# Optimization experiments

Measured on AMD Instinct MI355X. Metric: run time of the kernel, lower is better.

The kernel has to match this reference:

```python
import jax, jax.numpy as jnp
import numpy as np

B, LQ, H, NH, LK, N = 32, 256, 256, 8, 512, 8192
DH = H // NH
EPS = 1e-12

def layer_norm(x, g, b):
    m = x.mean(-1, keepdims=True)
    v = ((x - m) ** 2).mean(-1, keepdims=True)
    return (x - m) / jnp.sqrt(v + EPS) * g + b

def setup_inputs() -> dict:
    rs = np.random.RandomState(0)
    counts = rs.randint(LK // 2, LK + 1, size=B)  # ragged per-graph edge counts, max = LK
    E = int(counts.sum())
    edge_batch = jnp.asarray(np.repeat(np.arange(B), counts), jnp.int32)
    edge_pos = jnp.asarray(np.concatenate([np.arange(c) for c in counts]), jnp.int32)
    pad_mask = jnp.asarray((np.arange(LK)[None, :] < counts[:, None]).astype(np.float32))
    src = jnp.asarray(rs.randint(0, N, E), jnp.int32)
    dst = jnp.asarray(rs.randint(0, N, E), jnp.int32)
    ks = jax.random.split(jax.random.key(0), 16)
    def rn(i, shape, s=0.02):
        return jax.random.normal(ks[i], shape, jnp.float32) * s
    return dict(
        extended_attention_mask=jnp.zeros((B, 1, 1, LQ), jnp.float32),
        query=rn(0, (B, LQ, H), 1.0),
        rel_embedding_output=rn(1, (E, H), 1.0),
        graph_output=rn(2, (N, H), 1.0),
        src=src, dst=dst, edge_batch=edge_batch, edge_pos=edge_pos, pad_mask=pad_mask,
        Wq=rn(3, (H, H)), bq=jnp.zeros((H,), jnp.float32),
        Wk=rn(4, (2 * H, H)), bk=jnp.zeros((H,), jnp.float32),
        Wv=rn(5, (H, H)), bv=jnp.zeros((H,), jnp.float32),
        Wo=rn(6, (H, H)), bo=jnp.zeros((H,), jnp.float32),
        ln1_g=jnp.ones((H,), jnp.float32), ln1_b=jnp.zeros((H,), jnp.float32),
        W1=rn(7, (H, H)), b1=jnp.zeros((H,), jnp.float32),
        W2=rn(8, (H, H)), b2=jnp.zeros((H,), jnp.float32),
        ln2_g=jnp.ones((H,), jnp.float32), ln2_b=jnp.zeros((H,), jnp.float32),
    )

def reference(extended_attention_mask, query, rel_embedding_output, graph_output,
              src, dst, edge_batch, edge_pos, pad_mask,
              Wq, bq, Wk, bk, Wv, bv, Wo, bo, ln1_g, ln1_b,
              W1, b1, W2, b2, ln2_g, ln2_b):
    # --- memory_transform: edge gather + ragged pad (vectorized scatter) ---
    key_flat = jnp.concatenate([graph_output[src], rel_embedding_output], -1)  # [E, 2H]
    dst_flat = graph_output[dst]                                               # [E, H]
    key_pad = jnp.zeros((B, LK, 2 * H), key_flat.dtype).at[edge_batch, edge_pos].set(key_flat)
    val_pad = jnp.zeros((B, LK, H), dst_flat.dtype).at[edge_batch, edge_pos].set(dst_flat)
    cross_mask = (1.0 - pad_mask)[:, None, None, :] * -10000.0                 # [B,1,1,LK]
    # --- BidiAttention ---
    Q = (query @ Wq + bq).reshape(B, LQ, NH, DH)
    K = (key_pad @ Wk + bk).reshape(B, LK, NH, DH)
    V = (val_pad @ Wv + bv).reshape(B, LK, NH, DH)
    scores = jnp.einsum('bqhd,bkhd->bhqk', Q, K) / np.float32(np.sqrt(DH))
    pq = jax.nn.softmax(scores + cross_mask, axis=-1)
    query_ctx = jnp.einsum('bhqk,bkhd->bqhd', pq, V).reshape(B, LQ, H)
    pv = jax.nn.softmax(scores.transpose(0, 1, 3, 2) + extended_attention_mask, axis=-1)
    value_ctx = jnp.einsum('bhkq,bqhd->bkhd', pv, Q).reshape(B, LK, H)
    # --- RelAwareCross output / gate ---
    query_out = layer_norm(query_ctx @ Wo + bo + query, ln1_g, ln1_b)
    theta = jax.nn.sigmoid(value_ctx @ W1 + b1 + val_pad @ W2 + b2)
    value_new = layer_norm(theta * value_ctx + (1.0 - theta) * val_pad, ln2_g, ln2_b)
    # --- memory_update: unpad + scatter-mean by dst, replace rows with incoming edges ---
    val_edges = value_new[edge_batch, edge_pos]                                # [E, H]
    sums = jax.ops.segment_sum(val_edges, dst, num_segments=N)
    cnts = jax.ops.segment_sum(jnp.ones((val_edges.shape[0],), val_edges.dtype), dst, num_segments=N)
    mean = sums / jnp.maximum(cnts, 1.0)[:, None]
    graph_new = jnp.where((cnts > 0)[:, None], mean, graph_output)
    return (graph_new, query_out)
```

## Files before the change

### kernel.cpp

```cpp
#include <hip/hip_runtime.h>
#include <hip/hip_bf16.h>
#include <string.h>

#define B_ 32
#define LQ_ 256
#define H_ 256
#define NH_ 8
#define LK_ 512
#define N_ 8192
#define DH_ 32

typedef float floatx4 __attribute__((ext_vector_type(4)));
typedef short shortx8 __attribute__((ext_vector_type(8)));
typedef short shortx4 __attribute__((ext_vector_type(4)));

__device__ __forceinline__ short f2b(float f) {
    __hip_bfloat16 h = __float2bfloat16(f);
    short s;
    __builtin_memcpy(&s, &h, 2);
    return s;
}
__device__ __forceinline__ float b2f(short s) {
    unsigned u = ((unsigned)(unsigned short)s) << 16;
    float f;
    __builtin_memcpy(&f, &u, 4);
    return f;
}

#define LOG2E 1.44269504088896f
#define MFMA32(a, b, c) __builtin_amdgcn_mfma_f32_16x16x32_bf16(a, b, c, 0, 0, 0)
#define MFMA16(a, b, c) __builtin_amdgcn_mfma_f32_16x16x16bf16_1k(a, b, c, 0, 0, 0)

__global__ __launch_bounds__(256) void phase1(
    const float* __restrict__ graph, const float* __restrict__ rel,
    const int* __restrict__ src, const int* __restrict__ dst,
    const int* __restrict__ eb, const int* __restrict__ ep,
    const float* __restrict__ pad_mask,
    const float* __restrict__ Wq, const float* __restrict__ Wk,
    const float* __restrict__ Wv, const float* __restrict__ Wo,
    const float* __restrict__ W1, const float* __restrict__ W2,
    short* __restrict__ WT, short* __restrict__ key_pad,
    short* __restrict__ val_pad, int* __restrict__ head,
    int* __restrict__ row2e, int E) {
    const int bid = blockIdx.x, tid = threadIdx.x;
    if (bid < 8192) {
        int row = bid * 2 + (tid >> 7);
        int t = tid & 127;
        int b = row >> 9, p = row & 511;
        bool valid = pad_mask[row] > 0.5f;
        size_t krow = (size_t)row * 512;
        size_t vrow = (size_t)row * 256;
        int kc = t * 4, vc = t * 2;
        if (valid) {
            int lo = 0, hi = E;
            while (lo < hi) { int mid = (lo + hi) >> 1; if (eb[mid] < b) lo = mid + 1; else hi = mid; }
            int e = lo + p;
            int s = src[e], d = dst[e];
            const float* sp = (kc < 256) ? (graph + (size_t)s * 256 + kc)
                                         : (rel + (size_t)e * 256 + (kc - 256));
            float4 k4 = *(const float4*)sp;
            key_pad[krow + kc + 0] = f2b(k4.x);
            key_pad[krow + kc + 1] = f2b(k4.y);
            key_pad[krow + kc + 2] = f2b(k4.z);
            key_pad[krow + kc + 3] = f2b(k4.w);
            float2 v2 = *(const float2*)(graph + (size_t)d * 256 + vc);
            val_pad[vrow + vc + 0] = f2b(v2.x);
            val_pad[vrow + vc + 1] = f2b(v2.y);
        } else {
            *(long long*)&key_pad[krow + kc] = 0;
            *(int*)&val_pad[vrow + vc] = 0;
        }
    } else if (bid < 9984) {
        int i = (bid - 8192) * 256 + tid;
        const float* s;
        int K, loc;
        if (i < 65536) { s = Wq; K = 256; loc = i; }
        else if (i < 196608) { s = Wk; K = 512; loc = i - 65536; }
        else {
            int m = (i - 196608) >> 16;
            loc = (i - 196608) & 65535;
            K = 256;
            s = (m == 0) ? Wv : (m == 1) ? Wo : (m == 2) ? W1 : W2;
        }
        int n = loc / K, k = loc - n * K;
        WT[i] = f2b(s[(size_t)k * 256 + n]);
    } else {
        int i = (bid - 9984) * 256 + tid;
        if (i < 8192) head[i] = -1;
        for (int j = i; j < E; j += 8192)
            row2e[eb[j] * 512 + ep[j]] = j;
    }
}

__global__ __launch_bounds__(256) void phase2_gemm(
    const float* __restrict__ query, const short* __restrict__ key_pad,
    const short* __restrict__ val_pad, const short* __restrict__ WT,
    const float* __restrict__ bq, const float* __restrict__ bk,
    const float* __restrict__ bv,
    short* __restrict__ Qb, short* __restrict__ Kb,
    short* __restrict__ Vt, short* __restrict__ Qt) {
    __shared__ short As[128][40];
    __shared__ short Bs[128][40];
    const int tid = threadIdx.x;
    const int id = blockIdx.x;
    const float* Af = nullptr; const short* Ab = nullptr;
    const float* Bf = nullptr; const short* Bb = nullptr;
    const float* bias; short* C;
    size_t cbase; int cstride, K; bool biasM;
    if (id < 128) {
        int mt = id >> 1, nt = id & 1;
        Af = query + (size_t)(mt * 128) * 256; K = 256;
        Bb = WT + (size_t)(nt * 128) * 256;
        bias = bq + nt * 128; biasM = false;
        C = Qb; cbase = (size_t)(mt * 128) * 256 + nt * 128; cstride = 256;
    } else if (id < 384) {
        int t = id - 128; int mt = t >> 1, nt = t & 1;
        Ab = key_pad + (size_t)(mt * 128) * 512; K = 512;
        Bb = WT + 65536 + (size_t)(nt * 128) * 512;
        bias = bk + nt * 128; biasM = false;
        C = Kb; cbase = (size_t)(mt * 128) * 256 + nt * 128; cstride = 256;
    } else if (id < 640) {
        int t = id - 384; int b = t >> 3, ct = (t >> 2) & 1, nt = t & 3;
        Ab = WT + 196608 + (size_t)(ct * 128) * 256; K = 256;
        Bb = val_pad + ((size_t)(b * 512 + nt * 128)) * 256;
        bias = bv + ct * 128; biasM = true;
        C = Vt; cbase = ((size_t)(b * 256 + ct * 128)) * 512 + nt * 128; cstride = 512;
    } else {
        int t = id - 640; int b = t >> 2, ct = (t >> 1) & 1, qt = t & 1;
        Ab = WT + (size_t)(ct * 128) * 256; K = 256;
        Bf = query + ((size_t)(b * 256 + qt * 128)) * 256;
        bias = bq + ct * 128; biasM = true;
        C = Qt; cbase = ((size_t)(b * 256 + ct * 128)) * 256 + qt * 128; cstride = 256;
    }
    const int w = tid >> 6, lane = tid & 63;
    const int R0 = (w >> 1) * 64, C0 = (w & 1) * 64;
    const int lm = lane & 15, quad = lane >> 4;
    const int sr = tid >> 1, skq = (tid & 1) * 16;

    floatx4 acc[4][4];
#pragma unroll
    for (int i = 0; i < 4; i++)
#pragma unroll
        for (int j = 0; j < 4; j++) acc[i][j] = {0.f, 0.f, 0.f, 0.f};

    for (int kc = 0; kc < K; kc += 32) {
        if (Af) {
            const float* ap = Af + (size_t)sr * K + kc + skq;
            float4 a1 = *(const float4*)ap, a2 = *(const float4*)(ap + 4);
            float4 a3 = *(const float4*)(ap + 8), a4 = *(const float4*)(ap + 12);
            As[sr][skq + 0] = f2b(a1.x); As[sr][skq + 1] = f2b(a1.y);
            As[sr][skq + 2] = f2b(a1.z); As[sr][skq + 3] = f2b(a1.w);
            As[sr][skq + 4] = f2b(a2.x); As[sr][skq + 5] = f2b(a2.y);
            As[sr][skq + 6] = f2b(a2.z); As[sr][skq + 7] = f2b(a2.w);
            As[sr][skq + 8] = f2b(a3.x); As[sr][skq + 9] = f2b(a3.y);
            As[sr][skq + 10] = f2b(a3.z); As[sr][skq + 11] = f2b(a3.w);
            As[sr][skq + 12] = f2b(a4.x); As[sr][skq + 13] = f2b(a4.y);
            As[sr][skq + 14] = f2b(a4.z); As[sr][skq + 15] = f2b(a4.w);
        } else {
            const short* ap = Ab + (size_t)sr * K + kc + skq;
            *(shortx8*)&As[sr][skq] = *(const shortx8*)ap;
            *(shortx8*)&As[sr][skq + 8] = *(const shortx8*)(ap + 8);
        }
        if (Bf) {
            const float* bp = Bf + (size_t)sr * K + kc + skq;
            float4 a1 = *(const float4*)bp, a2 = *(const float4*)(bp + 4);
            float4 a3 = *(const float4*)(bp + 8), a4 = *(const float4*)(bp + 12);
            Bs[sr][skq + 0] = f2b(a1.x); Bs[sr][skq + 1] = f2b(a1.y);
            Bs[sr][skq + 2] = f2b(a1.z); Bs[sr][skq + 3] = f2b(a1.w);
            Bs[sr][skq + 4] = f2b(a2.x); Bs[sr][skq + 5] = f2b(a2.y);
            Bs[sr][skq + 6] = f2b(a2.z); Bs[sr][skq + 7] = f2b(a2.w);
            Bs[sr][skq + 8] = f2b(a3.x); Bs[sr][skq + 9] = f2b(a3.y);
            Bs[sr][skq + 10] = f2b(a3.z); Bs[sr][skq + 11] = f2b(a3.w);
            Bs[sr][skq + 12] = f2b(a4.x); Bs[sr][skq + 13] = f2b(a4.y);
            Bs[sr][skq + 14] = f2b(a4.z); Bs[sr][skq + 15] = f2b(a4.w);
        } else {
            const short* bp = Bb + (size_t)sr * K + kc + skq;
            *(shortx8*)&Bs[sr][skq] = *(const shortx8*)bp;
            *(shortx8*)&Bs[sr][skq + 8] = *(const shortx8*)(bp + 8);
        }
        __syncthreads();
        shortx8 af[4], bf[4];
#pragma unroll
        for (int i = 0; i < 4; i++) {
            af[i] = *(const shortx8*)&As[R0 + i * 16 + lm][quad * 8];
            bf[i] = *(const shortx8*)&Bs[C0 + i * 16 + lm][quad * 8];
        }
#pragma unroll
        for (int i = 0; i < 4; i++)
#pragma unroll
            for (int j = 0; j < 4; j++)
                acc[i][j] = MFMA32(af[i], bf[j], acc[i][j]);
        __syncthreads();
    }
#pragma unroll
    for (int i = 0; i < 4; i++) {
#pragma unroll
        for (int j = 0; j < 4; j++) {
            int gn = C0 + j * 16 + lm;
#pragma unroll
            for (int r = 0; r < 4; r++) {
                int gm = R0 + i * 16 + quad * 4 + r;
                float bvv = biasM ? bias[gm] : bias[gn];
                C[cbase + (size_t)gm * cstride + gn] = f2b(acc[i][j][r] + bvv);
            }
        }
    }
}

__global__ __launch_bounds__(512, 4) void phase3_attn(
    const short* __restrict__ Qm, const short* __restrict__ Km,
    const short* __restrict__ Vt, const short* __restrict__ Qt,
    const float* __restrict__ pad_mask, const float* __restrict__ ext,
    short* __restrict__ qctx, short* __restrict__ vctx) {
    __shared__ short SA[128][40];
    __shared__ short ST[32][136];
    const int tid = threadIdx.x;
    const int w = tid >> 6, lane = tid & 63;
    const int lm = lane & 15, quad = lane >> 4;
    const float scale2 = 0.17677669529663687f * LOG2E;
    const int id = blockIdx.x;

    if (id < 256) {
        const int b = id >> 3, h = id & 7;
        shortx8 bqf[2];
        bqf[0] = *(const shortx8*)(Qm + ((size_t)(b * 256 + w * 32 + lm)) * 256 + h * 32 + quad * 8);
        bqf[1] = *(const shortx8*)(Qm + ((size_t)(b * 256 + w * 32 + 16 + lm)) * 256 + h * 32 + quad * 8);
        floatx4 oacc[2][2] = {{{0.f,0.f,0.f,0.f},{0.f,0.f,0.f,0.f}},
                              {{0.f,0.f,0.f,0.f},{0.f,0.f,0.f,0.f}}};
        float psum[2] = {0.f, 0.f};
        const floatx4* pmp = (const floatx4*)(pad_mask + b * 512);
        for (int kc = 0; kc < 512; kc += 128) {
            if (tid < 256) {
                int r = tid >> 1, dq = (tid & 1) * 16;
                const short* kp = Km + ((size_t)(b * 512 + kc + r)) * 256 + h * 32 + dq;
                *(shortx8*)&SA[r][dq] = *(const shortx8*)kp;
                *(shortx8*)&SA[r][dq + 8] = *(const shortx8*)(kp + 8);
            } else {
                int u = tid - 256;
                int r = u >> 3, kq = (u & 7) * 16;
                const short* vp = Vt + ((size_t)(b * 256 + h * 32 + r)) * 512 + kc + kq;
                *(shortx8*)&ST[r][kq] = *(const shortx8*)vp;
                *(shortx8*)&ST[r][kq + 8] = *(const shortx8*)(vp + 8);
            }
            __syncthreads();
#pragma unroll
            for (int kh = 0; kh < 2; kh++) {
#pragma unroll
                for (int kt = 0; kt < 4; kt++) {
                    const int kw = kh * 64 + kt * 16;
                    shortx8 ak = *(const shortx8*)&SA[kw + lm][quad * 8];
                    floatx4 pm = pmp[kc / 4 + kh * 16 + kt * 4 + quad];
                    shortx4 av0 = *(const shortx4*)&ST[lm][kw + quad * 4];
                    shortx4 av1 = *(const shortx4*)&ST[16 + lm][kw + quad * 4];
#pragma unroll
                    for (int qf = 0; qf < 2; qf++) {
                        floatx4 s = {0.f, 0.f, 0.f, 0.f};
                        s = MFMA32(ak, bqf[qf], s);
                        shortx4 p4;
#pragma unroll
                        for (int r = 0; r < 4; r++) {
                            float e = __builtin_amdgcn_exp2f(
                                s[r] * scale2 + (1.0f - pm[r]) * (-10000.0f * LOG2E));
                            psum[qf] += e;
                            p4[r] = f2b(e);
                        }
                        oacc[qf][0] = MFMA16(av0, p4, oacc[qf][0]);
                        oacc[qf][1] = MFMA16(av1, p4, oacc[qf][1]);
                    }
                }
            }
            __syncthreads();
        }
#pragma unroll
        for (int qf = 0; qf < 2; qf++) {
            psum[qf] += __shfl_xor(psum[qf], 16, 64);
            psum[qf] += __shfl_xor(psum[qf], 32, 64);
            float inv = 1.0f / psum[qf];
            int q = w * 32 + qf * 16 + lm;
            short* op = qctx + ((size_t)(b * 256 + q)) * 256 + h * 32;
#pragma unroll
            for (int di = 0; di < 2; di++) {
                shortx4 o;
#pragma unroll
                for (int r = 0; r < 4; r++) o[r] = f2b(oacc[qf][di][r] * inv);
                *(long long*)(op + di * 16 + quad * 4) = *(long long*)&o;
            }
        }
    } else {
        const int t = id - 256;
        const int b = t >> 4, h = (t >> 1) & 7, khb = t & 1;
        shortx8 bkf[2];
        bkf[0] = *(const shortx8*)(Km + ((size_t)(b * 512 + khb * 256 + w * 32 + lm)) * 256 + h * 32 + quad * 8);
        bkf[1] = *(const shortx8*)(Km + ((size_t)(b * 512 + khb * 256 + w * 32 + 16 + lm)) * 256 + h * 32 + quad * 8);
        floatx4 oacc[2][2] = {{{0.f,0.f,0.f,0.f},{0.f,0.f,0.f,0.f}},
                              {{0.f,0.f,0.f,0.f},{0.f,0.f,0.f,0.f}}};
        float psum[2] = {0.f, 0.f};
        const floatx4* emp = (const floatx4*)(ext + b * 256);
        for (int qc = 0; qc < 256; qc += 128) {
            if (tid < 256) {
                int r = tid >> 1, dq = (tid & 1) * 16;
                const short* qp = Qm + ((size_t)(b * 256 + qc + r)) * 256 + h * 32 + dq;
                *(shortx8*)&SA[r][dq] = *(const shortx8*)qp;
                *(shortx8*)&SA[r][dq + 8] = *(const shortx8*)(qp + 8);
            } else {
                int u = tid - 256;
                int r = u >> 3, kq = (u & 7) * 16;
                const short* tp = Qt + ((size_t)(b * 256 + h * 32 + r)) * 256 + qc + kq;
                *(shortx8*)&ST[r][kq] = *(const shortx8*)tp;
                *(shortx8*)&ST[r][kq + 8] = *(const shortx8*)(tp + 8);
            }
            __syncthreads();
#pragma unroll
            for (int qh = 0; qh < 2; qh++) {
#pragma unroll
                for (int qt = 0; qt < 4; qt++) {
                    const int qw = qh * 64 + qt * 16;
                    shortx8 aq = *(const shortx8*)&SA[qw + lm][quad * 8];
                    floatx4 em = emp[qc / 4 + qh * 16 + qt * 4 + quad];
                    shortx4 av0 = *(const shortx4*)&ST[lm][qw + quad * 4];
                    shortx4 av1 = *(const shortx4*)&ST[16 + lm][qw + quad * 4];
#pragma unroll
                    for (int kf = 0; kf < 2; kf++) {
                        floatx4 s = {0.f, 0.f, 0.f, 0.f};
                        s = MFMA32(aq, bkf[kf], s);
                        shortx4 p4;
#pragma unroll
                        for (int r = 0; r < 4; r++) {
                            float e = __builtin_amdgcn_exp2f(s[r] * scale2 + em[r] * LOG2E);
                            psum[kf] += e;
                            p4[r] = f2b(e);
                        }
                        oacc[kf][0] = MFMA16(av0, p4, oacc[kf][0]);
                        oacc[kf][1] = MFMA16(av1, p4, oacc[kf][1]);
                    }
                }
            }
            __syncthreads();
        }
#pragma unroll
        for (int kf = 0; kf < 2; kf++) {
            psum[kf] += __shfl_xor(psum[kf], 16, 64);
            psum[kf] += __shfl_xor(psum[kf], 32, 64);
            float inv = 1.0f / psum[kf];
            int k = khb * 256 + w * 32 + kf * 16 + lm;
            short* op = vctx + ((size_t)(b * 512 + k)) * 256 + h * 32;
#pragma unroll
            for (int di = 0; di < 2; di++) {
                shortx4 o;
#pragma unroll
                for (int r = 0; r < 4; r++) o[r] = f2b(oacc[kf][di][r] * inv);
                *(long long*)(op + di * 16 + quad * 4) = *(long long*)&o;
            }
        }
    }
}

__global__ __launch_bounds__(256) void phase4a_gemm(
    const short* __restrict__ qctx, const short* __restrict__ vctx,
    const short* __restrict__ val_pad, const short* __restrict__ WTo,
    const short* __restrict__ WT1, const short* __restrict__ WT2,
    float* __restrict__ obuf, float* __restrict__ tbuf) {
    __shared__ short As[128][40];
    __shared__ short Bs[128][40];
    const int tid = threadIdx.x;
    const int id = blockIdx.x;
    const bool is_out = id < 128;
    int t = is_out ? id : id - 128;
    const int mt = t >> 1, nt = t & 1;
    const int w = tid >> 6, lane = tid & 63;
    const int R0 = (w >> 1) * 64, C0 = (w & 1) * 64;
    const int lm = lane & 15, quad = lane >> 4;
    const int sr = tid >> 1, skq = (tid & 1) * 16;
    const int npair = is_out ? 1 : 2;

    floatx4 acc[4][4];
#pragma unroll
    for (int i = 0; i < 4; i++)
#pragma unroll
        for (int j = 0; j < 4; j++) acc[i][j] = {0.f, 0.f, 0.f, 0.f};

    for (int pair = 0; pair < npair; pair++) {
        const short* Ap = is_out ? (qctx + (size_t)(mt * 128) * 256)
                                 : (pair == 0 ? vctx + (size_t)(mt * 128) * 256
                                              : val_pad + (size_t)(mt * 128) * 256);
        const short* Bp = is_out ? (WTo + (size_t)(nt * 128) * 256)
                                 : (pair == 0 ? WT1 + (size_t)(nt * 128) * 256
                                              : WT2 + (size_t)(nt * 128) * 256);
        for (int kc = 0; kc < 256; kc += 32) {
            const short* ap = Ap + (size_t)sr * 256 + kc + skq;
            *(shortx8*)&As[sr][skq] = *(const shortx8*)ap;
            *(shortx8*)&As[sr][skq + 8] = *(const shortx8*)(ap + 8);
            const short* bp = Bp + (size_t)sr * 256 + kc + skq;
            *(shortx8*)&Bs[sr][skq] = *(const shortx8*)bp;
            *(shortx8*)&Bs[sr][skq + 8] = *(const shortx8*)(bp + 8);
            __syncthreads();
            shortx8 af[4], bf[4];
#pragma unroll
            for (int i = 0; i < 4; i++) {
                af[i] = *(const shortx8*)&As[R0 + i * 16 + lm][quad * 8];
                bf[i] = *(const shortx8*)&Bs[C0 + i * 16 + lm][quad * 8];
            }
#pragma unroll
            for (int i = 0; i < 4; i++)
#pragma unroll
                for (int j = 0; j < 4; j++)
                    acc[i][j] = MFMA32(af[i], bf[j], acc[i][j]);
            __syncthreads();
        }
    }
    float* C = is_out ? obuf : tbuf;
    const size_t cbase = (size_t)(mt * 128) * 256 + nt * 128;
#pragma unroll
    for (int i = 0; i < 4; i++) {
#pragma unroll
        for (int j = 0; j < 4; j++) {
            int gn = C0 + j * 16 + lm;
#pragma unroll
            for (int r = 0; r < 4; r++) {
                int gm = R0 + i * 16 + quad * 4 + r;
                C[cbase + (size_t)gm * 256 + gn] = acc[i][j][r];
            }
        }
    }
}

__global__ __launch_bounds__(256) void phase4b_ln(
    const float* __restrict__ obuf, const float* __restrict__ bo,
    const float* __restrict__ query, const float* __restrict__ g1,
    const float* __restrict__ be1, float* __restrict__ out_q,
    float* __restrict__ tbuf, const short* __restrict__ vctx,
    const short* __restrict__ val_pad, const float* __restrict__ b1_,
    const float* __restrict__ b2_, const float* __restrict__ g2,
    const float* __restrict__ be2, const float* __restrict__ pad_mask,
    const int* __restrict__ row2e, const int* __restrict__ dst,
    int* __restrict__ head, int* __restrict__ nxt) {
    const int lane = threadIdx.x & 63, w = threadIdx.x >> 6;
    const int c0 = lane * 4;
    if (blockIdx.x < 2048) {
        int row = blockIdx.x * 4 + w;
        long long base = (long long)row * H_ + c0;
        float4 o = *(const float4*)(obuf + base);
        float4 bo4 = *(const float4*)(bo + c0);
        float4 q4 = *(const float4*)(query + base);
        float x0 = o.x + bo4.x + q4.x, x1 = o.y + bo4.y + q4.y;
        float x2 = o.z + bo4.z + q4.z, x3 = o.w + bo4.w + q4.w;
        float t = x0 + x1 + x2 + x3;
        for (int off = 32; off > 0; off >>= 1) t += __shfl_xor(t, off, 64);
        float mean = t * (1.0f / H_);
        float d0 = x0 - mean, d1 = x1 - mean, d2 = x2 - mean, d3 = x3 - mean;
        float v = d0 * d0 + d1 * d1 + d2 * d2 + d3 * d3;
        for (int off = 32; off > 0; off >>= 1) v += __shfl_xor(v, off, 64);
        float rs = rsqrtf(v * (1.0f / H_) + 1e-12f);
        float4 g = *(const float4*)(g1 + c0);
        float4 be = *(const float4*)(be1 + c0);
        float4 out;
        out.x = d0 * rs * g.x + be.x; out.y = d1 * rs * g.y + be.y;
        out.z = d2 * rs * g.z + be.z; out.w = d3 * rs * g.w + be.w;
        *(float4*)(out_q + base) = out;
    } else {
        int row = (blockIdx.x - 2048) * 4 + w;
        if (pad_mask[row] > 0.5f) {
            long long base = (long long)row * H_ + c0;
            float4 tb = *(const float4*)(tbuf + base);
            float4 b14 = *(const float4*)(b1_ + c0);
            float4 b24 = *(const float4*)(b2_ + c0);
            shortx4 vc = *(const shortx4*)(vctx + base);
            shortx4 vp = *(const shortx4*)(val_pad + base);
            float x[4];
#pragma unroll
            for (int j = 0; j < 4; j++) {
                float tv = (j == 0) ? tb.x : (j == 1) ? tb.y : (j == 2) ? tb.z : tb.w;
                float bb1 = (j == 0) ? b14.x : (j == 1) ? b14.y : (j == 2) ? b14.z : b14.w;
                float bb2 = (j == 0) ? b24.x : (j == 1) ? b24.y : (j == 2) ? b24.z : b24.w;
                float th = 1.0f / (1.0f + __expf(-(tv + bb1 + bb2)));
                x[j] = th * b2f(vc[j]) + (1.0f - th) * b2f(vp[j]);
            }
            float t = x[0] + x[1] + x[2] + x[3];
            for (int off = 32; off > 0; off >>= 1) t += __shfl_xor(t, off, 64);
            float mean = t * (1.0f / H_);
            float d0 = x[0] - mean, d1 = x[1] - mean, d2 = x[2] - mean, d3 = x[3] - mean;
            float v = d0 * d0 + d1 * d1 + d2 * d2 + d3 * d3;
            for (int off = 32; off > 0; off >>= 1) v += __shfl_xor(v, off, 64);
            float rs = rsqrtf(v * (1.0f / H_) + 1e-12f);
            float4 g = *(const float4*)(g2 + c0);
            float4 be = *(const float4*)(be2 + c0);
            float4 y4;
            y4.x = d0 * rs * g.x + be.x; y4.y = d1 * rs * g.y + be.y;
            y4.z = d2 * rs * g.z + be.z; y4.w = d3 * rs * g.w + be.w;
            *(float4*)(tbuf + base) = y4;
            if (lane == 0) {
                int d = dst[row2e[row]];
                int prev = atomicExch(&head[d], row);
                nxt[row] = prev;
            }
        }
    }
}

__global__ __launch_bounds__(256) void finalize_graph(
    const int* __restrict__ head, const int* __restrict__ nxt,
    const float* __restrict__ yrows, const float* __restrict__ graph,
    float* __restrict__ out_g) {
    int n = blockIdx.x, c = threadIdx.x;
    long long idx = (long long)n * H_ + c;
    int e = head[n];
    if (e < 0) { out_g[idx] = graph[idx]; return; }
    float acc = 0.f;
    int cnt = 0;
    while (e >= 0) {
        acc += yrows[(size_t)e * H_ + c];
        cnt++;
        e = nxt[e];
    }
    out_g[idx] = acc / (float)cnt;
}

extern "C" void kernel_launch(void* const* d_in, const int* in_sizes, int n_in,
                              void* d_out, int out_size, void* d_ws, size_t ws_size,
                              hipStream_t stream) {
    const float* ext_mask = (const float*)d_in[0];
    const float* query    = (const float*)d_in[1];
    const float* rel      = (const float*)d_in[2];
    const float* graph    = (const float*)d_in[3];
    const int*  src      = (const int*)d_in[4];
    const int*  dst      = (const int*)d_in[5];
    const int*  eb       = (const int*)d_in[6];
    const int*  ep       = (const int*)d_in[7];
    const float* pad_mask = (const float*)d_in[8];
    const float* Wq = (const float*)d_in[9];  const float* bq = (const float*)d_in[10];
    const float* Wk = (const float*)d_in[11]; const float* bk = (const float*)d_in[12];
    const float* Wv = (const float*)d_in[13]; const float* bv = (const float*)d_in[14];
    const float* Wo = (const float*)d_in[15]; const float* bo = (const float*)d_in[16];
    const float* g1 = (const float*)d_in[17]; const float* be1 = (const float*)d_in[18];
    const float* W1 = (const float*)d_in[19]; const float* b1 = (const float*)d_in[20];
    const float* W2 = (const float*)d_in[21]; const float* b2 = (const float*)d_in[22];
    const float* g2 = (const float*)d_in[23]; const float* be2 = (const float*)d_in[24];
    const int E = in_sizes[2] / H_;

    float* out_g = (float*)d_out;
    float* out_q = (float*)d_out + (size_t)N_ * H_;

    short* sp = (short*)d_ws;
    short* key_pad = sp; sp += (size_t)B_ * LK_ * 2 * H_;
    short* val_pad = sp; sp += (size_t)B_ * LK_ * H_;
    short* Qb      = sp; sp += (size_t)B_ * LQ_ * H_;
    short* Kb      = sp; sp += (size_t)B_ * LK_ * H_;
    short* Vt      = sp; sp += (size_t)B_ * H_ * LK_;
    short* Qt      = sp; sp += (size_t)B_ * H_ * LQ_;
    short* qctx    = sp; sp += (size_t)B_ * LQ_ * H_;
    short* vctx    = sp; sp += (size_t)B_ * LK_ * H_;
    short* WT      = sp; sp += 458752;
    short* WTo = WT + 262144;
    short* WT1 = WT + 327680;
    short* WT2 = WT + 393216;
    int* ip = (int*)(((size_t)sp + 15) & ~(size_t)15);
    int* head  = ip; ip += N_;
    int* nxt   = ip; ip += B_ * LK_;
    int* row2e = ip; ip += B_ * LK_;
    float* fp = (float*)ip;
    float* obuf = fp; fp += (size_t)B_ * LQ_ * H_;
    float* tbuf = fp; fp += (size_t)B_ * LK_ * H_;

    phase1<<<10016, 256, 0, stream>>>(graph, rel, src, dst, eb, ep, pad_mask,
                                      Wq, Wk, Wv, Wo, W1, W2,
                                      WT, key_pad, val_pad, head, row2e, E);
    phase2_gemm<<<768, 256, 0, stream>>>(query, key_pad, val_pad, WT,
                                         bq, bk, bv, Qb, Kb, Vt, Qt);
    phase3_attn<<<768, 512, 0, stream>>>(Qb, Kb, Vt, Qt, pad_mask, ext_mask,
                                         qctx, vctx);
    phase4a_gemm<<<384, 256, 0, stream>>>(qctx, vctx, val_pad, WTo, WT1, WT2,
                                          obuf, tbuf);
    phase4b_ln<<<6144, 256, 0, stream>>>(obuf, bo, query, g1, be1, out_q,
                                         tbuf, vctx, val_pad, b1, b2, g2, be2,
                                         pad_mask, row2e, dst, head, nxt);
    finalize_graph<<<N_, 256, 0, stream>>>(head, nxt, tbuf, graph, out_g);
}
```

Baseline: 237.7 us.

## Pre-convert query to bf16 and stage GEMM tiles via global_load_lds

Adds a phase1 block range that converts query to bf16 once. Both phase2 GEMM operands are then bf16, so tiles can be loaded straight into LDS with global_load_lds, 16 bytes per lane, in the phase2 and phase4a GEMMs. This removes the per-tile fp32-to-bf16 conversion that was repeated in every GEMM block and the register round trip for staging. In exchange it writes and reads an extra bf16 copy of query, and it drops the padded LDS rows (stride 32 instead of 40), which may cause bank conflicts on the fragment reads.

```diff
diff --git a/kernel.cpp b/kernel.cpp
--- a/kernel.cpp
+++ b/kernel.cpp
@@ -30,18 +30,21 @@
 #define LOG2E 1.44269504088896f
 #define MFMA32(a, b, c) __builtin_amdgcn_mfma_f32_16x16x32_bf16(a, b, c, 0, 0, 0)
 #define MFMA16(a, b, c) __builtin_amdgcn_mfma_f32_16x16x16bf16_1k(a, b, c, 0, 0, 0)
+typedef const __attribute__((address_space(1))) void* gptr_t;
+typedef __attribute__((address_space(3))) void* lptr_t;
+#define GLD16(g, l) __builtin_amdgcn_global_load_lds((gptr_t)(g), (lptr_t)(l), 16, 0, 0)
 
 __global__ __launch_bounds__(256) void phase1(
     const float* __restrict__ graph, const float* __restrict__ rel,
     const int* __restrict__ src, const int* __restrict__ dst,
     const int* __restrict__ eb, const int* __restrict__ ep,
-    const float* __restrict__ pad_mask,
+    const float* __restrict__ pad_mask, const float* __restrict__ query,
     const float* __restrict__ Wq, const float* __restrict__ Wk,
     const float* __restrict__ Wv, const float* __restrict__ Wo,
     const float* __restrict__ W1, const float* __restrict__ W2,
     short* __restrict__ WT, short* __restrict__ key_pad,
-    short* __restrict__ val_pad, int* __restrict__ head,
-    int* __restrict__ row2e, int E) {
+    short* __restrict__ val_pad, short* __restrict__ qbf,
+    int* __restrict__ head, int* __restrict__ row2e, int E) {
     const int bid = blockIdx.x, tid = threadIdx.x;
     if (bid < 8192) {
         int row = bid * 2 + (tid >> 7);
@@ -84,32 +87,42 @@
         }
         int n = loc / K, k = loc - n * K;
         WT[i] = f2b(s[(size_t)k * 256 + n]);
-    } else {
+    } else if (bid < 10016) {
         int i = (bid - 9984) * 256 + tid;
         if (i < 8192) head[i] = -1;
         for (int j = i; j < E; j += 8192)
             row2e[eb[j] * 512 + ep[j]] = j;
+    } else {
+        int i = (bid - 10016) * 256 + tid;
+        const float* qp = query + (size_t)i * 32;
+        short* op = qbf + (size_t)i * 32;
+#pragma unroll
+        for (int j = 0; j < 32; j += 4) {
+            float4 v = *(const float4*)(qp + j);
+            shortx4 o;
+            o[0] = f2b(v.x); o[1] = f2b(v.y); o[2] = f2b(v.z); o[3] = f2b(v.w);
+            *(long long*)(op + j) = *(long long*)&o;
+        }
     }
 }
 
 __global__ __launch_bounds__(256) void phase2_gemm(
-    const float* __restrict__ query, const short* __restrict__ key_pad,
+    const short* __restrict__ qbf, const short* __restrict__ key_pad,
     const short* __restrict__ val_pad, const short* __restrict__ WT,
     const float* __restrict__ bq, const float* __restrict__ bk,
     const float* __restrict__ bv,
     short* __restrict__ Qb, short* __restrict__ Kb,
     short* __restrict__ Vt, short* __restrict__ Qt) {
-    __shared__ short As[128][40];
-    __shared__ short Bs[128][40];
+    __shared__ short As[128 * 32];
+    __shared__ short Bs[128 * 32];
     const int tid = threadIdx.x;
     const int id = blockIdx.x;
-    const float* Af = nullptr; const short* Ab = nullptr;
-    const float* Bf = nullptr; const short* Bb = nullptr;
+    const short* Ab; const short* Bb;
     const float* bias; short* C;
     size_t cbase; int cstride, K; bool biasM;
     if (id < 128) {
         int mt = id >> 1, nt = id & 1;
-        Af = query + (size_t)(mt * 128) * 256; K = 256;
+        Ab = qbf + (size_t)(mt * 128) * 256; K = 256;
         Bb = WT + (size_t)(nt * 128) * 256;
         bias = bq + nt * 128; biasM = false;
         C = Qb; cbase = (size_t)(mt * 128) * 256 + nt * 128; cstride = 256;
@@ -128,14 +141,14 @@
     } else {
         int t = id - 640; int b = t >> 2, ct = (t >> 1) & 1, qt = t & 1;
         Ab = WT + (size_t)(ct * 128) * 256; K = 256;
-        Bf = query + ((size_t)(b * 256 + qt * 128)) * 256;
+        Bb = qbf + ((size_t)(b * 256 + qt * 128)) * 256;
         bias = bq + ct * 128; biasM = true;
         C = Qt; cbase = ((size_t)(b * 256 + ct * 128)) * 256 + qt * 128; cstride = 256;
     }
     const int w = tid >> 6, lane = tid & 63;
     const int R0 = (w >> 1) * 64, C0 = (w & 1) * 64;
     const int lm = lane & 15, quad = lane >> 4;
-    const int sr = tid >> 1, skq = (tid & 1) * 16;
+    const int srow = lane >> 2, scol = (lane & 3) * 8;
 
     floatx4 acc[4][4];
 #pragma unroll
@@ -144,46 +157,18 @@
         for (int j = 0; j < 4; j++) acc[i][j] = {0.f, 0.f, 0.f, 0.f};
 
     for (int kc = 0; kc < K; kc += 32) {
-        if (Af) {
-            const float* ap = Af + (size_t)sr * K + kc + skq;
-            float4 a1 = *(const float4*)ap, a2 = *(const float4*)(ap + 4);
-            float4 a3 = *(const float4*)(ap + 8), a4 = *(const float4*)(ap + 12);
-            As[sr][skq + 0] = f2b(a1.x); As[sr][skq + 1] = f2b(a1.y);
-            As[sr][skq + 2] = f2b(a1.z); As[sr][skq + 3] = f2b(a1.w);
-            As[sr][skq + 4] = f2b(a2.x); As[sr][skq + 5] = f2b(a2.y);
-            As[sr][skq + 6] = f2b(a2.z); As[sr][skq + 7] = f2b(a2.w);
-            As[sr][skq + 8] = f2b(a3.x); As[sr][skq + 9] = f2b(a3.y);
-            As[sr][skq + 10] = f2b(a3.z); As[sr][skq + 11] = f2b(a3.w);
-            As[sr][skq + 12] = f2b(a4.x); As[sr][skq + 13] = f2b(a4.y);
-            As[sr][skq + 14] = f2b(a4.z); As[sr][skq + 15] = f2b(a4.w);
-        } else {
-            const short* ap = Ab + (size_t)sr * K + kc + skq;
-            *(shortx8*)&As[sr][skq] = *(const shortx8*)ap;
-            *(shortx8*)&As[sr][skq + 8] = *(const shortx8*)(ap + 8);
-        }
-        if (Bf) {
-            const float* bp = Bf + (size_t)sr * K + kc + skq;
-            float4 a1 = *(const float4*)bp, a2 = *(const float4*)(bp + 4);
-            float4 a3 = *(const float4*)(bp + 8), a4 = *(const float4*)(bp + 12);
-            Bs[sr][skq + 0] = f2b(a1.x); Bs[sr][skq + 1] = f2b(a1.y);
-            Bs[sr][skq + 2] = f2b(a1.z); Bs[sr][skq + 3] = f2b(a1.w);
-            Bs[sr][skq + 4] = f2b(a2.x); Bs[sr][skq + 5] = f2b(a2.y);
-            Bs[sr][skq + 6] = f2b(a2.z); Bs[sr][skq + 7] = f2b(a2.w);
-            Bs[sr][skq + 8] = f2b(a3.x); Bs[sr][skq + 9] = f2b(a3.y);
-            Bs[sr][skq + 10] = f2b(a3.z); Bs[sr][skq + 11] = f2b(a3.w);
-            Bs[sr][skq + 12] = f2b(a4.x); Bs[sr][skq + 13] = f2b(a4.y);
-            Bs[sr][skq + 14] = f2b(a4.z); Bs[sr][skq + 15] = f2b(a4.w);
-        } else {
-            const short* bp = Bb + (size_t)sr * K + kc + skq;
-            *(shortx8*)&Bs[sr][skq] = *(const shortx8*)bp;
-            *(shortx8*)&Bs[sr][skq + 8] = *(const shortx8*)(bp + 8);
+#pragma unroll
+        for (int c = 0; c < 2; c++) {
+            const int row = w * 32 + c * 16;
+            GLD16(Ab + (size_t)(row + srow) * K + kc + scol, &As[row * 32]);
+            GLD16(Bb + (size_t)(row + srow) * K + kc + scol, &Bs[row * 32]);
         }
         __syncthreads();
         shortx8 af[4], bf[4];
 #pragma unroll
         for (int i = 0; i < 4; i++) {
-            af[i] = *(const shortx8*)&As[R0 + i * 16 + lm][quad * 8];
-            bf[i] = *(const shortx8*)&Bs[C0 + i * 16 + lm][quad * 8];
+            af[i] = *(const shortx8*)&As[(R0 + i * 16 + lm) * 32 + quad * 8];
+            bf[i] = *(const shortx8*)&Bs[(C0 + i * 16 + lm) * 32 + quad * 8];
         }
 #pragma unroll
         for (int i = 0; i < 4; i++)
@@ -360,8 +345,8 @@
     const short* __restrict__ val_pad, const short* __restrict__ WTo,
     const short* __restrict__ WT1, const short* __restrict__ WT2,
     float* __restrict__ obuf, float* __restrict__ tbuf) {
-    __shared__ short As[128][40];
-    __shared__ short Bs[128][40];
+    __shared__ short As[128 * 32];
+    __shared__ short Bs[128 * 32];
     const int tid = threadIdx.x;
     const int id = blockIdx.x;
     const bool is_out = id < 128;
@@ -370,7 +355,7 @@
     const int w = tid >> 6, lane = tid & 63;
     const int R0 = (w >> 1) * 64, C0 = (w & 1) * 64;
     const int lm = lane & 15, quad = lane >> 4;
-    const int sr = tid >> 1, skq = (tid & 1) * 16;
+    const int srow = lane >> 2, scol = (lane & 3) * 8;
     const int npair = is_out ? 1 : 2;
 
     floatx4 acc[4][4];
@@ -387,18 +372,18 @@
                                  : (pair == 0 ? WT1 + (size_t)(nt * 128) * 256
                                               : WT2 + (size_t)(nt * 128) * 256);
         for (int kc = 0; kc < 256; kc += 32) {
-            const short* ap = Ap + (size_t)sr * 256 + kc + skq;
-            *(shortx8*)&As[sr][skq] = *(const shortx8*)ap;
-            *(shortx8*)&As[sr][skq + 8] = *(const shortx8*)(ap + 8);
-            const short* bp = Bp + (size_t)sr * 256 + kc + skq;
-            *(shortx8*)&Bs[sr][skq] = *(const shortx8*)bp;
-            *(shortx8*)&Bs[sr][skq + 8] = *(const shortx8*)(bp + 8);
+#pragma unroll
+            for (int c = 0; c < 2; c++) {
+                const int row = w * 32 + c * 16;
+                GLD16(Ap + (size_t)(row + srow) * 256 + kc + scol, &As[row * 32]);
+                GLD16(Bp + (size_t)(row + srow) * 256 + kc + scol, &Bs[row * 32]);
+            }
             __syncthreads();
             shortx8 af[4], bf[4];
 #pragma unroll
             for (int i = 0; i < 4; i++) {
-                af[i] = *(const shortx8*)&As[R0 + i * 16 + lm][quad * 8];
-                bf[i] = *(const shortx8*)&Bs[C0 + i * 16 + lm][quad * 8];
+                af[i] = *(const shortx8*)&As[(R0 + i * 16 + lm) * 32 + quad * 8];
+                bf[i] = *(const shortx8*)&Bs[(C0 + i * 16 + lm) * 32 + quad * 8];
             }
 #pragma unroll
             for (int i = 0; i < 4; i++)
@@ -549,6 +534,7 @@
     short* Qt      = sp; sp += (size_t)B_ * H_ * LQ_;
     short* qctx    = sp; sp += (size_t)B_ * LQ_ * H_;
     short* vctx    = sp; sp += (size_t)B_ * LK_ * H_;
+    short* qbf     = sp; sp += (size_t)B_ * LQ_ * H_;
     short* WT      = sp; sp += 458752;
     short* WTo = WT + 262144;
     short* WT1 = WT + 327680;
@@ -561,10 +547,10 @@
     float* obuf = fp; fp += (size_t)B_ * LQ_ * H_;
     float* tbuf = fp; fp += (size_t)B_ * LK_ * H_;
 
-    phase1<<<10016, 256, 0, stream>>>(graph, rel, src, dst, eb, ep, pad_mask,
-                                      Wq, Wk, Wv, Wo, W1, W2,
-                                      WT, key_pad, val_pad, head, row2e, E);
-    phase2_gemm<<<768, 256, 0, stream>>>(query, key_pad, val_pad, WT,
+    phase1<<<10272, 256, 0, stream>>>(graph, rel, src, dst, eb, ep, pad_mask,
+                                      query, Wq, Wk, Wv, Wo, W1, W2,
+                                      WT, key_pad, val_pad, qbf, head, row2e, E);
+    phase2_gemm<<<768, 256, 0, stream>>>(qbf, key_pad, val_pad, WT,
                                          bq, bk, bv, Qb, Kb, Vt, Qt);
     phase3_attn<<<768, 512, 0, stream>>>(Qb, Kb, Vt, Qt, pad_mask, ext_mask,
                                          qctx, vctx);
```

Result: no change. 238.5 us (+0.3%).
